# Optimization experiments

Hardware: AMD Instinct MI355X
Metric: run time of the kernel (lower is better)

## Reference

```python
import jax, jax.numpy as jnp
import numpy as np

B, T, D, H = 2, 2048, 1024, 16
DH = D // H  # 64


def setup_inputs() -> dict:
    key = jax.random.key(0)
    ks = jax.random.split(key, 6)
    s = 1.0 / np.sqrt(D)
    return {
        "x": jax.random.normal(ks[0], (B, T, D), dtype=jnp.float32),
        "Wq": jax.random.normal(ks[1], (D, D), dtype=jnp.float32) * s,
        "Wk": jax.random.normal(ks[2], (D, D), dtype=jnp.float32) * s,
        "Wv": jax.random.normal(ks[3], (D, D), dtype=jnp.float32) * s,
        "Wo": jax.random.normal(ks[4], (D, D), dtype=jnp.float32) * s,
        "bo": jnp.zeros((D,), dtype=jnp.float32),
    }


def reference(x, Wq, Wk, Wv, Wo, bo):
    b, t, _ = x.shape
    # projections (torch Linear: x @ W.T; here W stored as [d_in, d_out])
    q = (x @ Wq).reshape(b, t, H, DH).transpose(0, 2, 1, 3)  # [b,H,t,dh]
    k = (x @ Wk).reshape(b, t, H, DH).transpose(0, 2, 1, 3)
    v = (x @ Wv).reshape(b, t, H, DH).transpose(0, 2, 1, 3)
    scores = jnp.einsum("bhqd,bhkd->bhqk", q, k) / np.sqrt(DH).astype(np.float32)
    causal = jnp.tril(jnp.ones((t, t), dtype=bool))  # True = keep
    scores = jnp.where(causal, scores, -jnp.inf)
    weights = jax.nn.softmax(scores, axis=-1)
    ctx = jnp.einsum("bhqk,bhkd->bhqd", weights, v)
    ctx = ctx.transpose(0, 2, 1, 3).reshape(b, t, D)
    return ctx @ Wo + bo
```

## Files before the change

kernel.cpp:

```cpp
#include <hip/hip_runtime.h>


typedef unsigned short u16;
typedef __attribute__((ext_vector_type(8))) short short8;
typedef __attribute__((ext_vector_type(4))) short short4_t;
typedef __attribute__((ext_vector_type(4))) float f32x4;

#define B_ 2
#define T_ 2048
#define D_ 1024
#define H_ 16
#define DH_ 64
#define M_ (B_ * T_)
#define SCALE_LOG2E 0.18033688011112042f
#define NEG_BIG -3.0e4f

#define GLOAD16(g, l)                                                     \
  __builtin_amdgcn_global_load_lds(                                       \
      (const __attribute__((address_space(1))) void*)(g),                 \
      (__attribute__((address_space(3))) void*)(l), 16, 0, 0)

__device__ __forceinline__ u16 f2bf(float f) {
  union { float f; unsigned u; } v; v.f = f;
  unsigned r = v.u + 0x7fffu + ((v.u >> 16) & 1u);
  return (u16)(r >> 16);
}
__device__ __forceinline__ u16 f2bf_trunc(float f) {
  union { float f; unsigned u; } v; v.f = f;
  return (u16)(v.u >> 16);
}
__device__ __forceinline__ float exp2_raw(float x) {
  float r;
  asm volatile("v_exp_f32 %0, %1" : "=v"(r) : "v"(x));
  return r;
}

__global__ __launch_bounds__(256) void cvt_x(const float* __restrict__ x,
                                             u16* __restrict__ xb) {
  const int i = (blockIdx.x * 256 + threadIdx.x) * 8;
  float4 a = *(const float4*)(x + i);
  float4 b = *(const float4*)(x + i + 4);
  short8 o;
  o[0] = (short)f2bf(a.x); o[1] = (short)f2bf(a.y);
  o[2] = (short)f2bf(a.z); o[3] = (short)f2bf(a.w);
  o[4] = (short)f2bf(b.x); o[5] = (short)f2bf(b.y);
  o[6] = (short)f2bf(b.z); o[7] = (short)f2bf(b.w);
  *(short8*)(xb + i) = o;
}

__global__ __launch_bounds__(256) void transpose_w(
    const float* __restrict__ w0, const float* __restrict__ w1,
    const float* __restrict__ w2, const float* __restrict__ w3,
    u16* __restrict__ outT) {
  __shared__ u16 Tl[64][72];
  const int z = blockIdx.z;
  const float* src = (z == 0) ? w0 : (z == 1) ? w1 : (z == 2) ? w2 : w3;
  const int r0 = blockIdx.y * 64, c0 = blockIdx.x * 64;
  const int tid = threadIdx.x;
  const int rr = tid >> 2, cc = (tid & 3) * 16;

  const float* p = src + (size_t)(r0 + rr) * D_ + c0 + cc;
  float4 f0 = *(const float4*)p;
  float4 f1 = *(const float4*)(p + 4);
  float4 f2 = *(const float4*)(p + 8);
  float4 f3 = *(const float4*)(p + 12);
  Tl[rr][cc + 0] = f2bf(f0.x); Tl[rr][cc + 1] = f2bf(f0.y);
  Tl[rr][cc + 2] = f2bf(f0.z); Tl[rr][cc + 3] = f2bf(f0.w);
  Tl[rr][cc + 4] = f2bf(f1.x); Tl[rr][cc + 5] = f2bf(f1.y);
  Tl[rr][cc + 6] = f2bf(f1.z); Tl[rr][cc + 7] = f2bf(f1.w);
  Tl[rr][cc + 8] = f2bf(f2.x); Tl[rr][cc + 9] = f2bf(f2.y);
  Tl[rr][cc +10] = f2bf(f2.z); Tl[rr][cc +11] = f2bf(f2.w);
  Tl[rr][cc +12] = f2bf(f3.x); Tl[rr][cc +13] = f2bf(f3.y);
  Tl[rr][cc +14] = f2bf(f3.z); Tl[rr][cc +15] = f2bf(f3.w);
  __syncthreads();

  u16* o = outT + (size_t)z * D_ * D_ + (size_t)(c0 + rr) * D_ + r0 + cc;
  short8 x0, x1;
#pragma unroll
  for (int i = 0; i < 8; i++) x0[i] = (short)Tl[cc + i][rr];
#pragma unroll
  for (int i = 0; i < 8; i++) x1[i] = (short)Tl[cc + 8 + i][rr];
  *(short8*)o = x0;
  *(short8*)(o + 8) = x1;
}

__global__ __launch_bounds__(256) void qkv_gemm(
    const u16* __restrict__ x, const u16* __restrict__ wT,
    u16* __restrict__ qkv) {
  __shared__ u16 As[128][32];
  __shared__ u16 Bs[128][32];

  const int z = blockIdx.z;
  const u16* W = wT + (size_t)z * D_ * D_;
  u16* out = qkv + (size_t)z * M_ * D_;
  const int n0 = blockIdx.x * 128;
  const int m0 = blockIdx.y * 128;
  const int tid = threadIdx.x;
  const int lane = tid & 63, w = tid >> 6;
  const int quad = lane >> 4, l16 = lane & 15;
  const int wr = w >> 1, wc = w & 1;

  f32x4 acc[4][4] = {};
  const int grow = w * 16 + (lane >> 2);
  const int gcol = (lane & 3) * 8;
  u16* lA = (u16*)As + w * 512;
  u16* lB = (u16*)Bs + w * 512;

  for (int k0 = 0; k0 < D_; k0 += 32) {
    const u16* gA = x + (size_t)(m0 + grow) * D_ + k0 + gcol;
    const u16* gB = W + (size_t)(n0 + grow) * D_ + k0 + gcol;
    GLOAD16(gA, lA);
    GLOAD16(gA + (size_t)64 * D_, lA + 2048);
    GLOAD16(gB, lB);
    GLOAD16(gB + (size_t)64 * D_, lB + 2048);
    __syncthreads();

    short8 af[4], bf[4];
#pragma unroll
    for (int i = 0; i < 4; i++)
      af[i] = *(const short8*)&As[wr * 64 + i * 16 + l16][quad * 8];
#pragma unroll
    for (int i = 0; i < 4; i++)
      bf[i] = *(const short8*)&Bs[wc * 64 + i * 16 + l16][quad * 8];
#pragma unroll
    for (int i = 0; i < 4; i++)
#pragma unroll
      for (int j = 0; j < 4; j++)
        acc[i][j] = __builtin_amdgcn_mfma_f32_16x16x32_bf16(af[i], bf[j], acc[i][j], 0, 0, 0);
    __syncthreads();
  }

  const float osc = (z == 0) ? SCALE_LOG2E : 1.0f;
#pragma unroll
  for (int i = 0; i < 4; i++) {
#pragma unroll
    for (int j = 0; j < 4; j++) {
      const int n = n0 + wc * 64 + j * 16 + l16;
      const int h = n >> 6, dh = n & 63;
#pragma unroll
      for (int r = 0; r < 4; r++) {
        const int m = m0 + wr * 64 + i * 16 + quad * 4 + r;
        const int b = m >> 11, t = m & (T_ - 1);
        out[(((size_t)(b * H_ + h)) * T_ + t) * DH_ + dh] = f2bf(acc[i][j][r] * osc);
      }
    }
  }
}

__global__ __launch_bounds__(256) void transpose_v(
    const u16* __restrict__ v, u16* __restrict__ vT) {
  __shared__ u16 Tl[64][72];
  const int t0 = blockIdx.x * 64;
  const int bh = blockIdx.y;
  const int tid = threadIdx.x;
  const int rr = tid >> 2, cc = (tid & 3) * 16;

  const u16* p = v + (size_t)bh * T_ * DH_ + (size_t)(t0 + rr) * DH_ + cc;
  short8 a0 = *(const short8*)p;
  short8 a1 = *(const short8*)(p + 8);
  *(short8*)&Tl[rr][cc] = a0;
  *(short8*)&Tl[rr][cc + 8] = a1;
  __syncthreads();

  u16* o = vT + (size_t)bh * DH_ * T_ + (size_t)rr * T_ + t0 + cc;
  short8 x0, x1;
#pragma unroll
  for (int i = 0; i < 8; i++) x0[i] = (short)Tl[cc + i][rr];
#pragma unroll
  for (int i = 0; i < 8; i++) x1[i] = (short)Tl[cc + 8 + i][rr];
  *(short8*)o = x0;
  *(short8*)(o + 8) = x1;
}

__global__ __launch_bounds__(128) void attn(
    const u16* __restrict__ qg, const u16* __restrict__ kg,
    const u16* __restrict__ vtg, u16* __restrict__ ctx) {
  __shared__ u16 Ks[64][72];
  __shared__ u16 Vs[64][72];
  __shared__ u16 Ps[2][2][16][72];

  const int qt = gridDim.x - 1 - blockIdx.x;
  const int bh = blockIdx.y;
  const int tid = threadIdx.x;
  const int w = tid >> 6, lane = tid & 63;
  const int quad = lane >> 4, l16 = lane & 15;
  const int q0 = qt * 64;
  const size_t baseQK = (size_t)bh * T_ * DH_;
  const size_t baseV  = (size_t)bh * DH_ * T_;

  const int qrowA = q0 + w * 32 + l16;
  const int qrowB = qrowA + 16;
  short8 qfA0 = *(const short8*)(qg + baseQK + (size_t)qrowA * DH_ + quad * 8);
  short8 qfA1 = *(const short8*)(qg + baseQK + (size_t)qrowA * DH_ + 32 + quad * 8);
  short8 qfB0 = *(const short8*)(qg + baseQK + (size_t)qrowB * DH_ + quad * 8);
  short8 qfB1 = *(const short8*)(qg + baseQK + (size_t)qrowB * DH_ + 32 + quad * 8);

  f32x4 oaccA[4] = {}, oaccB[4] = {};
  float liA = 0.f, liB = 0.f;

  const int srow = tid >> 1;
  const int scol = (tid & 1) * 32;

  const u16* kp = kg + baseQK + (size_t)srow * DH_ + scol;
  const u16* vp = vtg + baseV + (size_t)srow * T_ + scol;
  short8 kr0 = *(const short8*)kp;
  short8 kr1 = *(const short8*)(kp + 8);
  short8 kr2 = *(const short8*)(kp + 16);
  short8 kr3 = *(const short8*)(kp + 24);
  short8 vr0 = *(const short8*)vp;
  short8 vr1 = *(const short8*)(vp + 8);
  short8 vr2 = *(const short8*)(vp + 16);
  short8 vr3 = *(const short8*)(vp + 24);

  for (int kv0 = 0; kv0 <= q0; kv0 += 64) {
    __syncthreads();
    *(short8*)&Ks[srow][scol]      = kr0;
    *(short8*)&Ks[srow][scol + 8]  = kr1;
    *(short8*)&Ks[srow][scol + 16] = kr2;
    *(short8*)&Ks[srow][scol + 24] = kr3;
    *(short8*)&Vs[srow][scol]      = vr0;
    *(short8*)&Vs[srow][scol + 8]  = vr1;
    *(short8*)&Vs[srow][scol + 16] = vr2;
    *(short8*)&Vs[srow][scol + 24] = vr3;
    if (kv0 < q0) {
      const u16* kn = kg + baseQK + (size_t)(kv0 + 64 + srow) * DH_ + scol;
      const u16* vn = vtg + baseV + (size_t)srow * T_ + kv0 + 64 + scol;
      kr0 = *(const short8*)kn;
      kr1 = *(const short8*)(kn + 8);
      kr2 = *(const short8*)(kn + 16);
      kr3 = *(const short8*)(kn + 24);
      vr0 = *(const short8*)vn;
      vr1 = *(const short8*)(vn + 8);
      vr2 = *(const short8*)(vn + 16);
      vr3 = *(const short8*)(vn + 24);
    }
    __syncthreads();

    short8 kf0[4], kf1[4];
#pragma unroll
    for (int cb = 0; cb < 4; cb++) {
      kf0[cb] = *(const short8*)&Ks[cb * 16 + l16][quad * 8];
      kf1[cb] = *(const short8*)&Ks[cb * 16 + l16][32 + quad * 8];
    }

    f32x4 svA[4], svB[4];
#pragma unroll
    for (int cb = 0; cb < 4; cb++) {
      f32x4 z = {};
      svA[cb] = __builtin_amdgcn_mfma_f32_16x16x32_bf16(kf0[cb], qfA0, z, 0, 0, 0);
      svA[cb] = __builtin_amdgcn_mfma_f32_16x16x32_bf16(kf1[cb], qfA1, svA[cb], 0, 0, 0);
      svB[cb] = __builtin_amdgcn_mfma_f32_16x16x32_bf16(kf0[cb], qfB0, z, 0, 0, 0);
      svB[cb] = __builtin_amdgcn_mfma_f32_16x16x32_bf16(kf1[cb], qfB1, svB[cb], 0, 0, 0);
    }

    float pA[4][4], pB[4][4];
    if (kv0 == q0) {
#pragma unroll
      for (int cb = 0; cb < 4; cb++)
#pragma unroll
        for (int r = 0; r < 4; r++) {
          const int kv = kv0 + cb * 16 + quad * 4 + r;
          pA[cb][r] = exp2_raw((kv <= qrowA) ? svA[cb][r] : NEG_BIG);
          pB[cb][r] = exp2_raw((kv <= qrowB) ? svB[cb][r] : NEG_BIG);
        }
    } else {
#pragma unroll
      for (int cb = 0; cb < 4; cb++)
#pragma unroll
        for (int r = 0; r < 4; r++) {
          pA[cb][r] = exp2_raw(svA[cb][r]);
          pB[cb][r] = exp2_raw(svB[cb][r]);
        }
    }
#pragma unroll
    for (int cb = 0; cb < 4; cb++)
#pragma unroll
      for (int r = 0; r < 4; r++) { liA += pA[cb][r]; liB += pB[cb][r]; }

    short8 vf0[4], vf1[4];
#pragma unroll
    for (int cb = 0; cb < 4; cb++) {
      vf0[cb] = *(const short8*)&Vs[cb * 16 + l16][quad * 8];
      vf1[cb] = *(const short8*)&Vs[cb * 16 + l16][32 + quad * 8];
    }

#pragma unroll
    for (int cb = 0; cb < 4; cb++) {
      short4_t pkA, pkB;
#pragma unroll
      for (int r = 0; r < 4; r++) {
        pkA[r] = (short)f2bf_trunc(pA[cb][r]);
        pkB[r] = (short)f2bf_trunc(pB[cb][r]);
      }
      *(short4_t*)&Ps[w][0][l16][cb * 16 + quad * 4] = pkA;
      *(short4_t*)&Ps[w][1][l16][cb * 16 + quad * 4] = pkB;
    }
    short8 paA0 = *(const short8*)&Ps[w][0][l16][quad * 8];
    short8 paA1 = *(const short8*)&Ps[w][0][l16][32 + quad * 8];
    short8 paB0 = *(const short8*)&Ps[w][1][l16][quad * 8];
    short8 paB1 = *(const short8*)&Ps[w][1][l16][32 + quad * 8];
#pragma unroll
    for (int cb = 0; cb < 4; cb++) {
      oaccA[cb] = __builtin_amdgcn_mfma_f32_16x16x32_bf16(vf0[cb], paA0, oaccA[cb], 0, 0, 0);
      oaccA[cb] = __builtin_amdgcn_mfma_f32_16x16x32_bf16(vf1[cb], paA1, oaccA[cb], 0, 0, 0);
      oaccB[cb] = __builtin_amdgcn_mfma_f32_16x16x32_bf16(vf0[cb], paB0, oaccB[cb], 0, 0, 0);
      oaccB[cb] = __builtin_amdgcn_mfma_f32_16x16x32_bf16(vf1[cb], paB1, oaccB[cb], 0, 0, 0);
    }
  }

  liA += __shfl_xor(liA, 16, 64); liA += __shfl_xor(liA, 32, 64);
  liB += __shfl_xor(liB, 16, 64); liB += __shfl_xor(liB, 32, 64);
  const int b = bh >> 4, h = bh & 15;
  const float invA = 1.0f / liA, invB = 1.0f / liB;
  u16* outA = ctx + ((size_t)(b * T_ + qrowA)) * D_ + h * 64 + quad * 4;
  u16* outB = ctx + ((size_t)(b * T_ + qrowB)) * D_ + h * 64 + quad * 4;
#pragma unroll
  for (int cb = 0; cb < 4; cb++) {
    short4_t oA, oB;
#pragma unroll
    for (int r = 0; r < 4; r++) {
      oA[r] = (short)f2bf(oaccA[cb][r] * invA);
      oB[r] = (short)f2bf(oaccB[cb][r] * invB);
    }
    *(short4_t*)(outA + cb * 16) = oA;
    *(short4_t*)(outB + cb * 16) = oB;
  }
}

__global__ __launch_bounds__(256) void out_gemm(
    const u16* __restrict__ ctx, const u16* __restrict__ woT,
    const float* __restrict__ bo, float* __restrict__ out) {
  __shared__ u16 As[128][32];
  __shared__ u16 Bs[128][32];

  const int n0 = blockIdx.x * 128;
  const int m0 = blockIdx.y * 128;
  const int tid = threadIdx.x;
  const int lane = tid & 63, w = tid >> 6;
  const int quad = lane >> 4, l16 = lane & 15;
  const int wr = w >> 1, wc = w & 1;

  f32x4 acc[4][4] = {};
  const int grow = w * 16 + (lane >> 2);
  const int gcol = (lane & 3) * 8;
  u16* lA = (u16*)As + w * 512;
  u16* lB = (u16*)Bs + w * 512;

  for (int k0 = 0; k0 < D_; k0 += 32) {
    const u16* gA = ctx + (size_t)(m0 + grow) * D_ + k0 + gcol;
    const u16* gB = woT + (size_t)(n0 + grow) * D_ + k0 + gcol;
    GLOAD16(gA, lA);
    GLOAD16(gA + (size_t)64 * D_, lA + 2048);
    GLOAD16(gB, lB);
    GLOAD16(gB + (size_t)64 * D_, lB + 2048);
    __syncthreads();

    short8 af[4], bf[4];
#pragma unroll
    for (int i = 0; i < 4; i++)
      af[i] = *(const short8*)&As[wr * 64 + i * 16 + l16][quad * 8];
#pragma unroll
    for (int i = 0; i < 4; i++)
      bf[i] = *(const short8*)&Bs[wc * 64 + i * 16 + l16][quad * 8];
#pragma unroll
    for (int i = 0; i < 4; i++)
#pragma unroll
      for (int j = 0; j < 4; j++)
        acc[i][j] = __builtin_amdgcn_mfma_f32_16x16x32_bf16(af[i], bf[j], acc[i][j], 0, 0, 0);
    __syncthreads();
  }

#pragma unroll
  for (int i = 0; i < 4; i++) {
#pragma unroll
    for (int j = 0; j < 4; j++) {
      const int n = n0 + wc * 64 + j * 16 + l16;
      const float bias = bo[n];
#pragma unroll
      for (int r = 0; r < 4; r++) {
        const int m = m0 + wr * 64 + i * 16 + quad * 4 + r;
        out[(size_t)m * D_ + n] = acc[i][j][r] + bias;
      }
    }
  }
}

extern "C" void kernel_launch(void* const* d_in, const int* in_sizes, int n_in,
                              void* d_out, int out_size, void* d_ws, size_t ws_size,
                              hipStream_t stream) {
  const float* x  = (const float*)d_in[0];
  const float* Wq = (const float*)d_in[1];
  const float* Wk = (const float*)d_in[2];
  const float* Wv = (const float*)d_in[3];
  const float* Wo = (const float*)d_in[4];
  const float* bo = (const float*)d_in[5];
  float* out = (float*)d_out;

  u16* ws  = (u16*)d_ws;
  u16* xb  = ws;
  u16* wT  = xb + (size_t)M_ * D_;
  u16* qkv = wT + (size_t)4 * D_ * D_;
  u16* ctx = qkv + (size_t)3 * M_ * D_;
  u16* vT  = xb;

  cvt_x<<<dim3(M_ * D_ / (256 * 8)), 256, 0, stream>>>(x, xb);
  transpose_w<<<dim3(16, 16, 4), 256, 0, stream>>>(Wq, Wk, Wv, Wo, wT);
  qkv_gemm<<<dim3(D_ / 128, M_ / 128, 3), 256, 0, stream>>>(xb, wT, qkv);
  transpose_v<<<dim3(T_ / 64, B_ * H_), 256, 0, stream>>>(qkv + (size_t)2 * M_ * D_, vT);
  attn<<<dim3(T_ / 64, B_ * H_), 128, 0, stream>>>(
      qkv, qkv + (size_t)M_ * D_, vT, ctx);
  out_gemm<<<dim3(D_ / 128, M_ / 128), 256, 0, stream>>>(ctx, wT + (size_t)3 * D_ * D_, bo, out);
}
```

Before: 207.1 us.

## Double-buffer K/V in attention, reuse P scratch, halve out_gemm M tile

```diff
diff --git a/kernel.cpp b/kernel.cpp
--- a/kernel.cpp
+++ b/kernel.cpp
@@ -175,9 +175,9 @@
 __global__ __launch_bounds__(128) void attn(
     const u16* __restrict__ qg, const u16* __restrict__ kg,
     const u16* __restrict__ vtg, u16* __restrict__ ctx) {
-  __shared__ u16 Ks[64][72];
-  __shared__ u16 Vs[64][72];
-  __shared__ u16 Ps[2][2][16][72];
+  __shared__ u16 Ks[2][64][72];
+  __shared__ u16 Vs[2][64][72];
+  __shared__ u16 Ps[2][16][72];
 
   const int qt = gridDim.x - 1 - blockIdx.x;
   const int bh = blockIdx.y;
@@ -201,46 +201,64 @@
   const int srow = tid >> 1;
   const int scol = (tid & 1) * 32;
 
-  const u16* kp = kg + baseQK + (size_t)srow * DH_ + scol;
-  const u16* vp = vtg + baseV + (size_t)srow * T_ + scol;
-  short8 kr0 = *(const short8*)kp;
-  short8 kr1 = *(const short8*)(kp + 8);
-  short8 kr2 = *(const short8*)(kp + 16);
-  short8 kr3 = *(const short8*)(kp + 24);
-  short8 vr0 = *(const short8*)vp;
-  short8 vr1 = *(const short8*)(vp + 8);
-  short8 vr2 = *(const short8*)(vp + 16);
-  short8 vr3 = *(const short8*)(vp + 24);
-
-  for (int kv0 = 0; kv0 <= q0; kv0 += 64) {
+  short8 kr0, kr1, kr2, kr3, vr0, vr1, vr2, vr3;
+  {
+    const u16* kp = kg + baseQK + (size_t)srow * DH_ + scol;
+    const u16* vp = vtg + baseV + (size_t)srow * T_ + scol;
+    short8 a0 = *(const short8*)kp;
+    short8 a1 = *(const short8*)(kp + 8);
+    short8 a2 = *(const short8*)(kp + 16);
+    short8 a3 = *(const short8*)(kp + 24);
+    short8 b0 = *(const short8*)vp;
+    short8 b1 = *(const short8*)(vp + 8);
+    short8 b2 = *(const short8*)(vp + 16);
+    short8 b3 = *(const short8*)(vp + 24);
+    *(short8*)&Ks[0][srow][scol]      = a0;
+    *(short8*)&Ks[0][srow][scol + 8]  = a1;
+    *(short8*)&Ks[0][srow][scol + 16] = a2;
+    *(short8*)&Ks[0][srow][scol + 24] = a3;
+    *(short8*)&Vs[0][srow][scol]      = b0;
+    *(short8*)&Vs[0][srow][scol + 8]  = b1;
+    *(short8*)&Vs[0][srow][scol + 16] = b2;
+    *(short8*)&Vs[0][srow][scol + 24] = b3;
+  }
+  if (q0 >= 64) {
+    const u16* kn = kg + baseQK + (size_t)(64 + srow) * DH_ + scol;
+    const u16* vn = vtg + baseV + (size_t)srow * T_ + 64 + scol;
+    kr0 = *(const short8*)kn; kr1 = *(const short8*)(kn + 8);
+    kr2 = *(const short8*)(kn + 16); kr3 = *(const short8*)(kn + 24);
+    vr0 = *(const short8*)vn; vr1 = *(const short8*)(vn + 8);
+    vr2 = *(const short8*)(vn + 16); vr3 = *(const short8*)(vn + 24);
+  }
+
+  int buf = 0;
+  for (int kv0 = 0; kv0 <= q0; kv0 += 64, buf ^= 1) {
     __syncthreads();
-    *(short8*)&Ks[srow][scol]      = kr0;
-    *(short8*)&Ks[srow][scol + 8]  = kr1;
-    *(short8*)&Ks[srow][scol + 16] = kr2;
-    *(short8*)&Ks[srow][scol + 24] = kr3;
-    *(short8*)&Vs[srow][scol]      = vr0;
-    *(short8*)&Vs[srow][scol + 8]  = vr1;
-    *(short8*)&Vs[srow][scol + 16] = vr2;
-    *(short8*)&Vs[srow][scol + 24] = vr3;
-    if (kv0 < q0) {
-      const u16* kn = kg + baseQK + (size_t)(kv0 + 64 + srow) * DH_ + scol;
-      const u16* vn = vtg + baseV + (size_t)srow * T_ + kv0 + 64 + scol;
-      kr0 = *(const short8*)kn;
-      kr1 = *(const short8*)(kn + 8);
-      kr2 = *(const short8*)(kn + 16);
-      kr3 = *(const short8*)(kn + 24);
-      vr0 = *(const short8*)vn;
-      vr1 = *(const short8*)(vn + 8);
-      vr2 = *(const short8*)(vn + 16);
-      vr3 = *(const short8*)(vn + 24);
-    }
-    __syncthreads();
+
+    if (kv0 + 64 <= q0) {
+      *(short8*)&Ks[buf ^ 1][srow][scol]      = kr0;
+      *(short8*)&Ks[buf ^ 1][srow][scol + 8]  = kr1;
+      *(short8*)&Ks[buf ^ 1][srow][scol + 16] = kr2;
+      *(short8*)&Ks[buf ^ 1][srow][scol + 24] = kr3;
+      *(short8*)&Vs[buf ^ 1][srow][scol]      = vr0;
+      *(short8*)&Vs[buf ^ 1][srow][scol + 8]  = vr1;
+      *(short8*)&Vs[buf ^ 1][srow][scol + 16] = vr2;
+      *(short8*)&Vs[buf ^ 1][srow][scol + 24] = vr3;
+      if (kv0 + 128 <= q0) {
+        const u16* kn = kg + baseQK + (size_t)(kv0 + 128 + srow) * DH_ + scol;
+        const u16* vn = vtg + baseV + (size_t)srow * T_ + kv0 + 128 + scol;
+        kr0 = *(const short8*)kn; kr1 = *(const short8*)(kn + 8);
+        kr2 = *(const short8*)(kn + 16); kr3 = *(const short8*)(kn + 24);
+        vr0 = *(const short8*)vn; vr1 = *(const short8*)(vn + 8);
+        vr2 = *(const short8*)(vn + 16); vr3 = *(const short8*)(vn + 24);
+      }
+    }
 
     short8 kf0[4], kf1[4];
 #pragma unroll
     for (int cb = 0; cb < 4; cb++) {
-      kf0[cb] = *(const short8*)&Ks[cb * 16 + l16][quad * 8];
-      kf1[cb] = *(const short8*)&Ks[cb * 16 + l16][32 + quad * 8];
+      kf0[cb] = *(const short8*)&Ks[buf][cb * 16 + l16][quad * 8];
+      kf1[cb] = *(const short8*)&Ks[buf][cb * 16 + l16][32 + quad * 8];
     }
 
     f32x4 svA[4], svB[4];
@@ -280,29 +298,36 @@
     short8 vf0[4], vf1[4];
 #pragma unroll
     for (int cb = 0; cb < 4; cb++) {
-      vf0[cb] = *(const short8*)&Vs[cb * 16 + l16][quad * 8];
-      vf1[cb] = *(const short8*)&Vs[cb * 16 + l16][32 + quad * 8];
-    }
-
-#pragma unroll
-    for (int cb = 0; cb < 4; cb++) {
-      short4_t pkA, pkB;
-#pragma unroll
-      for (int r = 0; r < 4; r++) {
-        pkA[r] = (short)f2bf_trunc(pA[cb][r]);
-        pkB[r] = (short)f2bf_trunc(pB[cb][r]);
-      }
-      *(short4_t*)&Ps[w][0][l16][cb * 16 + quad * 4] = pkA;
-      *(short4_t*)&Ps[w][1][l16][cb * 16 + quad * 4] = pkB;
-    }
-    short8 paA0 = *(const short8*)&Ps[w][0][l16][quad * 8];
-    short8 paA1 = *(const short8*)&Ps[w][0][l16][32 + quad * 8];
-    short8 paB0 = *(const short8*)&Ps[w][1][l16][quad * 8];
-    short8 paB1 = *(const short8*)&Ps[w][1][l16][32 + quad * 8];
+      vf0[cb] = *(const short8*)&Vs[buf][cb * 16 + l16][quad * 8];
+      vf1[cb] = *(const short8*)&Vs[buf][cb * 16 + l16][32 + quad * 8];
+    }
+
+#pragma unroll
+    for (int cb = 0; cb < 4; cb++) {
+      short4_t pk;
+#pragma unroll
+      for (int r = 0; r < 4; r++) pk[r] = (short)f2bf_trunc(pA[cb][r]);
+      *(short4_t*)&Ps[w][l16][cb * 16 + quad * 4] = pk;
+    }
+    short8 paA0 = *(const short8*)&Ps[w][l16][quad * 8];
+    short8 paA1 = *(const short8*)&Ps[w][l16][32 + quad * 8];
 #pragma unroll
     for (int cb = 0; cb < 4; cb++) {
       oaccA[cb] = __builtin_amdgcn_mfma_f32_16x16x32_bf16(vf0[cb], paA0, oaccA[cb], 0, 0, 0);
       oaccA[cb] = __builtin_amdgcn_mfma_f32_16x16x32_bf16(vf1[cb], paA1, oaccA[cb], 0, 0, 0);
+    }
+
+#pragma unroll
+    for (int cb = 0; cb < 4; cb++) {
+      short4_t pk;
+#pragma unroll
+      for (int r = 0; r < 4; r++) pk[r] = (short)f2bf_trunc(pB[cb][r]);
+      *(short4_t*)&Ps[w][l16][cb * 16 + quad * 4] = pk;
+    }
+    short8 paB0 = *(const short8*)&Ps[w][l16][quad * 8];
+    short8 paB1 = *(const short8*)&Ps[w][l16][32 + quad * 8];
+#pragma unroll
+    for (int cb = 0; cb < 4; cb++) {
       oaccB[cb] = __builtin_amdgcn_mfma_f32_16x16x32_bf16(vf0[cb], paB0, oaccB[cb], 0, 0, 0);
       oaccB[cb] = __builtin_amdgcn_mfma_f32_16x16x32_bf16(vf1[cb], paB1, oaccB[cb], 0, 0, 0);
     }
@@ -330,17 +355,17 @@
 __global__ __launch_bounds__(256) void out_gemm(
     const u16* __restrict__ ctx, const u16* __restrict__ woT,
     const float* __restrict__ bo, float* __restrict__ out) {
-  __shared__ u16 As[128][32];
+  __shared__ u16 As[64][32];
   __shared__ u16 Bs[128][32];
 
   const int n0 = blockIdx.x * 128;
-  const int m0 = blockIdx.y * 128;
+  const int m0 = blockIdx.y * 64;
   const int tid = threadIdx.x;
   const int lane = tid & 63, w = tid >> 6;
   const int quad = lane >> 4, l16 = lane & 15;
   const int wr = w >> 1, wc = w & 1;
 
-  f32x4 acc[4][4] = {};
+  f32x4 acc[2][4] = {};
   const int grow = w * 16 + (lane >> 2);
   const int gcol = (lane & 3) * 8;
   u16* lA = (u16*)As + w * 512;
@@ -350,20 +375,19 @@
     const u16* gA = ctx + (size_t)(m0 + grow) * D_ + k0 + gcol;
     const u16* gB = woT + (size_t)(n0 + grow) * D_ + k0 + gcol;
     GLOAD16(gA, lA);
-    GLOAD16(gA + (size_t)64 * D_, lA + 2048);
     GLOAD16(gB, lB);
     GLOAD16(gB + (size_t)64 * D_, lB + 2048);
     __syncthreads();
 
-    short8 af[4], bf[4];
-#pragma unroll
-    for (int i = 0; i < 4; i++)
-      af[i] = *(const short8*)&As[wr * 64 + i * 16 + l16][quad * 8];
+    short8 af[2], bf[4];
+#pragma unroll
+    for (int i = 0; i < 2; i++)
+      af[i] = *(const short8*)&As[wr * 32 + i * 16 + l16][quad * 8];
 #pragma unroll
     for (int i = 0; i < 4; i++)
       bf[i] = *(const short8*)&Bs[wc * 64 + i * 16 + l16][quad * 8];
 #pragma unroll
-    for (int i = 0; i < 4; i++)
+    for (int i = 0; i < 2; i++)
 #pragma unroll
       for (int j = 0; j < 4; j++)
         acc[i][j] = __builtin_amdgcn_mfma_f32_16x16x32_bf16(af[i], bf[j], acc[i][j], 0, 0, 0);
@@ -371,14 +395,14 @@
   }
 
 #pragma unroll
-  for (int i = 0; i < 4; i++) {
+  for (int i = 0; i < 2; i++) {
 #pragma unroll
     for (int j = 0; j < 4; j++) {
       const int n = n0 + wc * 64 + j * 16 + l16;
       const float bias = bo[n];
 #pragma unroll
       for (int r = 0; r < 4; r++) {
-        const int m = m0 + wr * 64 + i * 16 + quad * 4 + r;
+        const int m = m0 + wr * 32 + i * 16 + quad * 4 + r;
         out[(size_t)m * D_ + n] = acc[i][j][r] + bias;
       }
     }
@@ -409,5 +433,5 @@
   transpose_v<<<dim3(T_ / 64, B_ * H_), 256, 0, stream>>>(qkv + (size_t)2 * M_ * D_, vT);
   attn<<<dim3(T_ / 64, B_ * H_), 128, 0, stream>>>(
       qkv, qkv + (size_t)M_ * D_, vT, ctx);
-  out_gemm<<<dim3(D_ / 128, M_ / 128), 256, 0, stream>>>(ctx, wT + (size_t)3 * D_ * D_, bo, out);
-}
+  out_gemm<<<dim3(D_ / 128, M_ / 64), 256, 0, stream>>>(ctx, wT + (size_t)3 * D_ * D_, bo, out);
+}
```

Result: slower. 238.8 us (+15.3%).
